# Kernel tuning notes

Measured on AMD Instinct MI355X. Metric: run time of the kernel, lower is better.

Reference implementation:

```python
import jax, jax.numpy as jnp
import numpy as np

NUM_EXPERTS = 8
TOP_K = 2
HIDDEN = 1024
INTER = 3584
BATCH = 2
SEQ = 2048
TOKENS = BATCH * SEQ


def setup_inputs() -> dict:
    key = jax.random.key(0)
    k_h, k_l, k_w1, k_w2, k_w3 = jax.random.split(key, 5)
    hidden_states = jax.random.normal(k_h, (TOKENS, HIDDEN), dtype=jnp.float32)
    # Router: top-2 over softmaxed logits, renormalized (standard Mixtral routing)
    logits = jax.random.normal(k_l, (TOKENS, NUM_EXPERTS), dtype=jnp.float32)
    probs = jax.nn.softmax(logits, axis=-1)
    routing_weights, selected = jax.lax.top_k(probs, TOP_K)  # [T, K], [T, K]
    routing_weights = routing_weights / jnp.sum(routing_weights, axis=-1, keepdims=True)
    # expert_mask: [num_experts, top_k, tokens]
    expert_mask = jax.nn.one_hot(selected, NUM_EXPERTS, dtype=jnp.int32).transpose(2, 1, 0)
    scale = 0.02
    w1 = jax.random.normal(k_w1, (NUM_EXPERTS, HIDDEN, INTER), dtype=jnp.float32) * scale
    w2 = jax.random.normal(k_w2, (NUM_EXPERTS, INTER, HIDDEN), dtype=jnp.float32) * scale
    w3 = jax.random.normal(k_w3, (NUM_EXPERTS, HIDDEN, INTER), dtype=jnp.float32) * scale
    return {
        "expert_mask": expert_mask,
        "hidden_states": hidden_states,
        "routing_weights": routing_weights,
        "w1": w1,
        "w2": w2,
        "w3": w3,
        "batch_size": BATCH,
        "sequence_length": SEQ,
        "hidden_dim": HIDDEN,
    }


def reference(expert_mask, hidden_states, routing_weights, w1, w2, w3,
              batch_size, sequence_length, hidden_dim):
    num_experts = w1.shape[0]
    tokens = batch_size * sequence_length
    # Extra row at the end absorbs writes from fill_value=-1 padding (as in source).
    final = jnp.zeros((tokens + 1, hidden_dim), dtype=hidden_states.dtype)
    for e in range(num_experts):
        # idx: which top-k slot; top_x: which token. Padded with -1.
        idx, top_x = jnp.nonzero(expert_mask[e], size=sequence_length, fill_value=-1)
        cur = hidden_states[top_x]  # [S, H]
        h = (jax.nn.silu(cur @ w1[e]) * (cur @ w3[e])) @ w2[e]  # SwiGLU MLP
        h = h * routing_weights[top_x, idx, None]
        final = final.at[top_x].set(h + final[top_x])
    final = final[:-1]
    return final.reshape(batch_size, sequence_length, hidden_dim)
```

## Files before the change

### kernel.cpp

```cpp
#include <hip/hip_runtime.h>
#include <hip/hip_bf16.h>
#include <cstdint>
#include <cstddef>

#define NEXP  8
#define NTOK  4096
#define HID   1024
#define INTER 3584
#define CAP   2048

#define BM  128
#define BN  128
#define BK  32
#define BKP 40

typedef __attribute__((ext_vector_type(4))) float floatx4;
typedef __attribute__((ext_vector_type(8))) short shortx8;

__device__ __forceinline__ unsigned short f2bf(float f) {
    union { float f; unsigned u; } v; v.f = f;
    unsigned r = v.u + 0x7fffu + ((v.u >> 16) & 1u);
    return (unsigned short)(r >> 16);
}

__device__ __forceinline__ shortx8 pack8(const float* v) {
    shortx8 r;
#pragma unroll
    for (int i = 0; i < 8; ++i) r[i] = (short)f2bf(v[i]);
    return r;
}

__global__ void route_kernel(const int* __restrict__ mask, const float* __restrict__ rw,
                             int* __restrict__ cnt, int* __restrict__ list,
                             float* __restrict__ wgt) {
    int t = blockIdx.x * blockDim.x + threadIdx.x;
    if (t >= NTOK) return;
#pragma unroll
    for (int e = 0; e < NEXP; ++e) {
#pragma unroll
        for (int k = 0; k < 2; ++k) {
            if (mask[(e * 2 + k) * NTOK + t] != 0) {
                int pos = atomicAdd(&cnt[e], 1);
                if (pos < CAP) {
                    list[e * CAP + pos] = t;
                    wgt[e * CAP + pos] = rw[t * 2 + k];
                }
            }
        }
    }
}

__global__ __launch_bounds__(256, 2)
void gemm1_kernel(const float* __restrict__ X, const float* __restrict__ W1,
                  const float* __restrict__ W3, const int* __restrict__ cnt,
                  const int* __restrict__ list, const float* __restrict__ wgt,
                  unsigned short* __restrict__ H) {
    const int e  = blockIdx.z;
    const int ce = min(cnt[e], CAP);
    const int m0 = blockIdx.y * BM;
    if (m0 >= ce) return;
    const int n0 = blockIdx.x * BN;

    __shared__ unsigned short lds_a [BM * BKP];
    __shared__ unsigned short lds_w1[BN * BKP];
    __shared__ unsigned short lds_w3[BN * BKP];

    const int tid = threadIdx.x;
    const int am = tid >> 1;
    const int ah = tid & 1;
    const int tok = list[e * CAP + min(m0 + am, ce - 1)];
    const float* xp = X + (size_t)tok * HID;
    const int wn = tid & 127;
    const int wk = tid >> 7;
    const float* w1base = W1 + (size_t)e * HID * INTER + n0 + wn;
    const float* w3base = W3 + (size_t)e * HID * INTER + n0 + wn;

    const int lane = tid & 63;
    const int wave = tid >> 6;
    const int wm  = (wave >> 1) * 64;
    const int wnn = (wave & 1) * 64;
    const int fl  = lane & 15;
    const int fq  = lane >> 4;

    floatx4 acc1[4][4], acc3[4][4];
#pragma unroll
    for (int i = 0; i < 4; ++i)
#pragma unroll
        for (int j = 0; j < 4; ++j)
#pragma unroll
            for (int r = 0; r < 4; ++r) { acc1[i][j][r] = 0.f; acc3[i][j][r] = 0.f; }

    for (int k0 = 0; k0 < HID; k0 += BK) {
        __syncthreads();
        {
            const float* s = xp + k0 + ah * 16;
            float v[16];
#pragma unroll
            for (int i = 0; i < 4; ++i) {
                float4 f = ((const float4*)s)[i];
                v[4*i+0]=f.x; v[4*i+1]=f.y; v[4*i+2]=f.z; v[4*i+3]=f.w;
            }
            shortx8* dst = (shortx8*)&lds_a[am * BKP + ah * 16];
            dst[0] = pack8(v);
            dst[1] = pack8(v + 8);
        }
#pragma unroll
        for (int p = 0; p < 2; ++p) {
            const int kk = p * 16 + wk * 8;
            {
                const float* s = w1base + (size_t)(k0 + kk) * INTER;
                float v[8];
#pragma unroll
                for (int i = 0; i < 8; ++i) v[i] = s[(size_t)i * INTER];
                *(shortx8*)&lds_w1[wn * BKP + kk] = pack8(v);
            }
            {
                const float* s = w3base + (size_t)(k0 + kk) * INTER;
                float v[8];
#pragma unroll
                for (int i = 0; i < 8; ++i) v[i] = s[(size_t)i * INTER];
                *(shortx8*)&lds_w3[wn * BKP + kk] = pack8(v);
            }
        }
        __syncthreads();

        shortx8 af[4], b1[4], b3[4];
#pragma unroll
        for (int i = 0; i < 4; ++i)
            af[i] = *(const shortx8*)&lds_a[(wm + i * 16 + fl) * BKP + fq * 8];
#pragma unroll
        for (int j = 0; j < 4; ++j) {
            b1[j] = *(const shortx8*)&lds_w1[(wnn + j * 16 + fl) * BKP + fq * 8];
            b3[j] = *(const shortx8*)&lds_w3[(wnn + j * 16 + fl) * BKP + fq * 8];
        }
#pragma unroll
        for (int i = 0; i < 4; ++i)
#pragma unroll
            for (int j = 0; j < 4; ++j) {
                acc1[i][j] = __builtin_amdgcn_mfma_f32_16x16x32_bf16(af[i], b1[j], acc1[i][j], 0, 0, 0);
                acc3[i][j] = __builtin_amdgcn_mfma_f32_16x16x32_bf16(af[i], b3[j], acc3[i][j], 0, 0, 0);
            }
    }

#pragma unroll
    for (int i = 0; i < 4; ++i) {
        const int rowb = m0 + wm + i * 16 + fq * 4;
#pragma unroll
        for (int r = 0; r < 4; ++r) {
            const int row = rowb + r;
            const bool valid = row < ce;
            const float rwv = valid ? wgt[e * CAP + row] : 0.f;
            unsigned short* hp = H + (size_t)(e * CAP + (valid ? row : 0)) * INTER;
#pragma unroll
            for (int j = 0; j < 4; ++j) {
                const int col = n0 + wnn + j * 16 + fl;
                float h1 = acc1[i][j][r];
                float h3 = acc3[i][j][r];
                float sv = h1 / (1.f + __expf(-h1)) * h3 * rwv;
                if (valid) hp[col] = f2bf(sv);
            }
        }
    }
}

__global__ __launch_bounds__(256, 2)
void gemm2_kernel(const unsigned short* __restrict__ H, const float* __restrict__ W2,
                  const int* __restrict__ cnt, const int* __restrict__ list,
                  float* __restrict__ out) {
    const int e  = blockIdx.z;
    const int ce = min(cnt[e], CAP);
    const int m0 = blockIdx.y * BM;
    if (m0 >= ce) return;
    const int n0 = blockIdx.x * BN;

    __shared__ unsigned short lds_a[BM * BKP];
    __shared__ unsigned short lds_w[BN * BKP];

    const int tid = threadIdx.x;
    const int am = tid >> 1;
    const int ah = tid & 1;
    const int arow = min(m0 + am, ce - 1);
    const unsigned short* hp = H + (size_t)(e * CAP + arow) * INTER;

    const int wn = tid & 127;
    const int wk = tid >> 7;
    const float* w2base = W2 + (size_t)e * INTER * HID + n0 + wn;

    const int lane = tid & 63;
    const int wave = tid >> 6;
    const int wm  = (wave >> 1) * 64;
    const int wnn = (wave & 1) * 64;
    const int fl  = lane & 15;
    const int fq  = lane >> 4;

    floatx4 acc[4][4];
#pragma unroll
    for (int i = 0; i < 4; ++i)
#pragma unroll
        for (int j = 0; j < 4; ++j)
#pragma unroll
            for (int r = 0; r < 4; ++r) acc[i][j][r] = 0.f;

    for (int k0 = 0; k0 < INTER; k0 += BK) {
        __syncthreads();
        {
            const shortx8* s = (const shortx8*)(hp + k0 + ah * 16);
            shortx8 v0 = s[0], v1 = s[1];
            shortx8* dst = (shortx8*)&lds_a[am * BKP + ah * 16];
            dst[0] = v0; dst[1] = v1;
        }
#pragma unroll
        for (int p = 0; p < 2; ++p) {
            const int kk = p * 16 + wk * 8;
            const float* s = w2base + (size_t)(k0 + kk) * HID;
            float v[8];
#pragma unroll
            for (int i = 0; i < 8; ++i) v[i] = s[(size_t)i * HID];
            *(shortx8*)&lds_w[wn * BKP + kk] = pack8(v);
        }
        __syncthreads();

        shortx8 af[4], bf[4];
#pragma unroll
        for (int i = 0; i < 4; ++i)
            af[i] = *(const shortx8*)&lds_a[(wm + i * 16 + fl) * BKP + fq * 8];
#pragma unroll
        for (int j = 0; j < 4; ++j)
            bf[j] = *(const shortx8*)&lds_w[(wnn + j * 16 + fl) * BKP + fq * 8];
#pragma unroll
        for (int i = 0; i < 4; ++i)
#pragma unroll
            for (int j = 0; j < 4; ++j)
                acc[i][j] = __builtin_amdgcn_mfma_f32_16x16x32_bf16(af[i], bf[j], acc[i][j], 0, 0, 0);
    }

#pragma unroll
    for (int i = 0; i < 4; ++i) {
        const int rowb = m0 + wm + i * 16 + fq * 4;
#pragma unroll
        for (int r = 0; r < 4; ++r) {
            const int row = rowb + r;
            const bool valid = row < ce;
            const int tok = valid ? list[e * CAP + row] : 0;
            float* op = out + (size_t)tok * HID;
#pragma unroll
            for (int j = 0; j < 4; ++j) {
                const int col = n0 + wnn + j * 16 + fl;
                if (valid) atomicAdd(&op[col], acc[i][j][r]);
            }
        }
    }
}

extern "C" void kernel_launch(void* const* d_in, const int* in_sizes, int n_in,
                              void* d_out, int out_size, void* d_ws, size_t ws_size,
                              hipStream_t stream) {
    const int*   mask = (const int*)  d_in[0];
    const float* X    = (const float*)d_in[1];
    const float* rw   = (const float*)d_in[2];
    const float* w1   = (const float*)d_in[3];
    const float* w2   = (const float*)d_in[4];
    const float* w3   = (const float*)d_in[5];
    float* out = (float*)d_out;

    char* ws = (char*)d_ws;
    int*   cnt  = (int*)ws;
    int*   list = (int*)(ws + 256);
    float* wgt  = (float*)(ws + 256 + 65536);
    unsigned short* H = (unsigned short*)(ws + 256 + 131072);

    hipMemsetAsync(cnt, 0, 256, stream);
    hipMemsetAsync(d_out, 0, (size_t)out_size * sizeof(float), stream);

    route_kernel<<<dim3((NTOK + 255) / 256), dim3(256), 0, stream>>>(mask, rw, cnt, list, wgt);
    gemm1_kernel<<<dim3(INTER / BN, CAP / BM, NEXP), dim3(256), 0, stream>>>(X, w1, w3, cnt, list, wgt, H);
    gemm2_kernel<<<dim3(HID / BN, CAP / BM, NEXP), dim3(256), 0, stream>>>(H, w2, cnt, list, out);
}
```

Measured before the change: 762.1 us.

## Pre-convert weights to transposed bf16 and use async global-to-LDS loads

Adds per-call pre-pass kernels that convert X to bf16 and transpose-convert W1, W3 and W2 to K-contiguous bf16 layouts in workspace. Both GEMMs then fill their LDS tiles with 16-byte direct global-to-LDS loads instead of strided fp32 loads followed by in-register conversion. The aim is to halve weight traffic inside the GEMMs and drop the conversion ALU work from their inner loops. In exchange, every call pays a full fp32 read and bf16 write of all weights, and the LDS tiles lose their padding, which may cause bank conflicts.

```diff
diff --git a/kernel.cpp b/kernel.cpp
--- a/kernel.cpp
+++ b/kernel.cpp
@@ -12,15 +12,15 @@
 #define BM  128
 #define BN  128
 #define BK  32
-#define BKP 40
 
 typedef __attribute__((ext_vector_type(4))) float floatx4;
 typedef __attribute__((ext_vector_type(8))) short shortx8;
-
-__device__ __forceinline__ unsigned short f2bf(float f) {
+typedef unsigned short u16;
+
+__device__ __forceinline__ u16 f2bf(float f) {
     union { float f; unsigned u; } v; v.f = f;
     unsigned r = v.u + 0x7fffu + ((v.u >> 16) & 1u);
-    return (unsigned short)(r >> 16);
+    return (u16)(r >> 16);
 }
 
 __device__ __forceinline__ shortx8 pack8(const float* v) {
@@ -28,6 +28,12 @@
 #pragma unroll
     for (int i = 0; i < 8; ++i) r[i] = (short)f2bf(v[i]);
     return r;
+}
+
+__device__ __forceinline__ void async_ld16(const void* g, void* l) {
+    __builtin_amdgcn_global_load_lds(
+        (const __attribute__((address_space(1))) unsigned int*)g,
+        (__attribute__((address_space(3))) unsigned int*)l, 16, 0, 0);
 }
 
 __global__ void route_kernel(const int* __restrict__ mask, const float* __restrict__ rw,
@@ -50,37 +56,82 @@
     }
 }
 
+__global__ void xcvt_kernel(const float* __restrict__ X, u16* __restrict__ Xb) {
+    const int i = (blockIdx.x * 256 + threadIdx.x) * 8;
+    float4 a = *(const float4*)&X[i];
+    float4 b = *(const float4*)&X[i + 4];
+    float v[8] = {a.x, a.y, a.z, a.w, b.x, b.y, b.z, b.w};
+    *(shortx8*)&Xb[i] = pack8(v);
+}
+
+__global__ void transpose_cvt_kernel(const float* __restrict__ src, u16* __restrict__ dst,
+                                     int K, int N) {
+    const int e = blockIdx.z;
+    src += (size_t)e * K * N;
+    dst += (size_t)e * K * N;
+    const int n0 = blockIdx.x * 64;
+    const int k0 = blockIdx.y * 64;
+    __shared__ u16 lds[64 * 72];
+    const int t  = threadIdx.x;
+    const int rr = t >> 4;
+    const int c4 = t & 15;
+#pragma unroll
+    for (int it = 0; it < 4; ++it) {
+        const int r = it * 16 + rr;
+        float4 f = *(const float4*)&src[(size_t)(k0 + r) * N + n0 + c4 * 4];
+        lds[(c4 * 4 + 0) * 72 + r] = f2bf(f.x);
+        lds[(c4 * 4 + 1) * 72 + r] = f2bf(f.y);
+        lds[(c4 * 4 + 2) * 72 + r] = f2bf(f.z);
+        lds[(c4 * 4 + 3) * 72 + r] = f2bf(f.w);
+    }
+    __syncthreads();
+    const int row8 = t >> 3;
+    const int col8 = t & 7;
+#pragma unroll
+    for (int it = 0; it < 2; ++it) {
+        const int row = it * 32 + row8;
+        *(shortx8*)&dst[(size_t)(n0 + row) * K + k0 + col8 * 8] =
+            *(const shortx8*)&lds[row * 72 + col8 * 8];
+    }
+}
+
 __global__ __launch_bounds__(256, 2)
-void gemm1_kernel(const float* __restrict__ X, const float* __restrict__ W1,
-                  const float* __restrict__ W3, const int* __restrict__ cnt,
+void gemm1_kernel(const u16* __restrict__ Xb, const u16* __restrict__ W1b,
+                  const u16* __restrict__ W3b, const int* __restrict__ cnt,
                   const int* __restrict__ list, const float* __restrict__ wgt,
-                  unsigned short* __restrict__ H) {
+                  u16* __restrict__ H) {
     const int e  = blockIdx.z;
     const int ce = min(cnt[e], CAP);
     const int m0 = blockIdx.y * BM;
     if (m0 >= ce) return;
     const int n0 = blockIdx.x * BN;
 
-    __shared__ unsigned short lds_a [BM * BKP];
-    __shared__ unsigned short lds_w1[BN * BKP];
-    __shared__ unsigned short lds_w3[BN * BKP];
-
-    const int tid = threadIdx.x;
-    const int am = tid >> 1;
-    const int ah = tid & 1;
-    const int tok = list[e * CAP + min(m0 + am, ce - 1)];
-    const float* xp = X + (size_t)tok * HID;
-    const int wn = tid & 127;
-    const int wk = tid >> 7;
-    const float* w1base = W1 + (size_t)e * HID * INTER + n0 + wn;
-    const float* w3base = W3 + (size_t)e * HID * INTER + n0 + wn;
-
+    __shared__ u16 lA [BM * BK];
+    __shared__ u16 lB1[BN * BK];
+    __shared__ u16 lB3[BN * BK];
+
+    const int tid  = threadIdx.x;
     const int lane = tid & 63;
     const int wave = tid >> 6;
+
+    const int srow0 = wave * 32 + (lane >> 2);
+    const int srow1 = srow0 + 16;
+    const int scol  = (lane & 3) * 8;
+    const int lo0 = wave * 1024 + lane * 8;
+    const int lo1 = lo0 + 512;
+
+    const int t0 = list[e * CAP + min(m0 + srow0, ce - 1)];
+    const int t1 = list[e * CAP + min(m0 + srow1, ce - 1)];
+    const u16* ap0  = Xb + (size_t)t0 * HID + scol;
+    const u16* ap1  = Xb + (size_t)t1 * HID + scol;
+    const u16* b1p0 = W1b + ((size_t)e * INTER + n0 + srow0) * HID + scol;
+    const u16* b1p1 = b1p0 + (size_t)16 * HID;
+    const u16* b3p0 = W3b + ((size_t)e * INTER + n0 + srow0) * HID + scol;
+    const u16* b3p1 = b3p0 + (size_t)16 * HID;
+
+    const int fl = lane & 15, fq = lane >> 4;
     const int wm  = (wave >> 1) * 64;
     const int wnn = (wave & 1) * 64;
-    const int fl  = lane & 15;
-    const int fq  = lane >> 4;
 
     floatx4 acc1[4][4], acc3[4][4];
 #pragma unroll
@@ -92,53 +143,29 @@
 
     for (int k0 = 0; k0 < HID; k0 += BK) {
         __syncthreads();
-        {
-            const float* s = xp + k0 + ah * 16;
-            float v[16];
-#pragma unroll
-            for (int i = 0; i < 4; ++i) {
-                float4 f = ((const float4*)s)[i];
-                v[4*i+0]=f.x; v[4*i+1]=f.y; v[4*i+2]=f.z; v[4*i+3]=f.w;
-            }
-            shortx8* dst = (shortx8*)&lds_a[am * BKP + ah * 16];
-            dst[0] = pack8(v);
-            dst[1] = pack8(v + 8);
+        async_ld16(ap0  + k0, &lA [lo0]);
+        async_ld16(ap1  + k0, &lA [lo1]);
+        async_ld16(b1p0 + k0, &lB1[lo0]);
+        async_ld16(b1p1 + k0, &lB1[lo1]);
+        async_ld16(b3p0 + k0, &lB3[lo0]);
+        async_ld16(b3p1 + k0, &lB3[lo1]);
+        __syncthreads();
+
+        shortx8 af[4], b1f[4], b3f[4];
+#pragma unroll
+        for (int i = 0; i < 4; ++i)
+            af[i] = *(const shortx8*)&lA[(wm + i * 16 + fl) * BK + fq * 8];
+#pragma unroll
+        for (int j = 0; j < 4; ++j) {
+            b1f[j] = *(const shortx8*)&lB1[(wnn + j * 16 + fl) * BK + fq * 8];
+            b3f[j] = *(const shortx8*)&lB3[(wnn + j * 16 + fl) * BK + fq * 8];
         }
 #pragma unroll
-        for (int p = 0; p < 2; ++p) {
-            const int kk = p * 16 + wk * 8;
-            {
-                const float* s = w1base + (size_t)(k0 + kk) * INTER;
-                float v[8];
-#pragma unroll
-                for (int i = 0; i < 8; ++i) v[i] = s[(size_t)i * INTER];
-                *(shortx8*)&lds_w1[wn * BKP + kk] = pack8(v);
-            }
-            {
-                const float* s = w3base + (size_t)(k0 + kk) * INTER;
-                float v[8];
-#pragma unroll
-                for (int i = 0; i < 8; ++i) v[i] = s[(size_t)i * INTER];
-                *(shortx8*)&lds_w3[wn * BKP + kk] = pack8(v);
-            }
-        }
-        __syncthreads();
-
-        shortx8 af[4], b1[4], b3[4];
-#pragma unroll
         for (int i = 0; i < 4; ++i)
-            af[i] = *(const shortx8*)&lds_a[(wm + i * 16 + fl) * BKP + fq * 8];
-#pragma unroll
-        for (int j = 0; j < 4; ++j) {
-            b1[j] = *(const shortx8*)&lds_w1[(wnn + j * 16 + fl) * BKP + fq * 8];
-            b3[j] = *(const shortx8*)&lds_w3[(wnn + j * 16 + fl) * BKP + fq * 8];
-        }
-#pragma unroll
-        for (int i = 0; i < 4; ++i)
 #pragma unroll
             for (int j = 0; j < 4; ++j) {
-                acc1[i][j] = __builtin_amdgcn_mfma_f32_16x16x32_bf16(af[i], b1[j], acc1[i][j], 0, 0, 0);
-                acc3[i][j] = __builtin_amdgcn_mfma_f32_16x16x32_bf16(af[i], b3[j], acc3[i][j], 0, 0, 0);
+                acc1[i][j] = __builtin_amdgcn_mfma_f32_16x16x32_bf16(af[i], b1f[j], acc1[i][j], 0, 0, 0);
+                acc3[i][j] = __builtin_amdgcn_mfma_f32_16x16x32_bf16(af[i], b3f[j], acc3[i][j], 0, 0, 0);
             }
     }
 
@@ -150,7 +177,7 @@
             const int row = rowb + r;
             const bool valid = row < ce;
             const float rwv = valid ? wgt[e * CAP + row] : 0.f;
-            unsigned short* hp = H + (size_t)(e * CAP + (valid ? row : 0)) * INTER;
+            u16* hp = H + (size_t)(e * CAP + (valid ? row : 0)) * INTER;
 #pragma unroll
             for (int j = 0; j < 4; ++j) {
                 const int col = n0 + wnn + j * 16 + fl;
@@ -164,7 +191,7 @@
 }
 
 __global__ __launch_bounds__(256, 2)
-void gemm2_kernel(const unsigned short* __restrict__ H, const float* __restrict__ W2,
+void gemm2_kernel(const u16* __restrict__ H, const u16* __restrict__ W2b,
                   const int* __restrict__ cnt, const int* __restrict__ list,
                   float* __restrict__ out) {
     const int e  = blockIdx.z;
@@ -173,25 +200,27 @@
     if (m0 >= ce) return;
     const int n0 = blockIdx.x * BN;
 
-    __shared__ unsigned short lds_a[BM * BKP];
-    __shared__ unsigned short lds_w[BN * BKP];
-
-    const int tid = threadIdx.x;
-    const int am = tid >> 1;
-    const int ah = tid & 1;
-    const int arow = min(m0 + am, ce - 1);
-    const unsigned short* hp = H + (size_t)(e * CAP + arow) * INTER;
-
-    const int wn = tid & 127;
-    const int wk = tid >> 7;
-    const float* w2base = W2 + (size_t)e * INTER * HID + n0 + wn;
-
+    __shared__ u16 lA[BM * BK];
+    __shared__ u16 lB[BN * BK];
+
+    const int tid  = threadIdx.x;
     const int lane = tid & 63;
     const int wave = tid >> 6;
+
+    const int srow0 = wave * 32 + (lane >> 2);
+    const int srow1 = srow0 + 16;
+    const int scol  = (lane & 3) * 8;
+    const int lo0 = wave * 1024 + lane * 8;
+    const int lo1 = lo0 + 512;
+
+    const u16* ap0 = H + (size_t)(e * CAP + m0 + srow0) * INTER + scol;
+    const u16* ap1 = ap0 + (size_t)16 * INTER;
+    const u16* bp0 = W2b + ((size_t)e * HID + n0 + srow0) * INTER + scol;
+    const u16* bp1 = bp0 + (size_t)16 * INTER;
+
+    const int fl = lane & 15, fq = lane >> 4;
     const int wm  = (wave >> 1) * 64;
     const int wnn = (wave & 1) * 64;
-    const int fl  = lane & 15;
-    const int fq  = lane >> 4;
 
     floatx4 acc[4][4];
 #pragma unroll
@@ -203,30 +232,19 @@
 
     for (int k0 = 0; k0 < INTER; k0 += BK) {
         __syncthreads();
-        {
-            const shortx8* s = (const shortx8*)(hp + k0 + ah * 16);
-            shortx8 v0 = s[0], v1 = s[1];
-            shortx8* dst = (shortx8*)&lds_a[am * BKP + ah * 16];
-            dst[0] = v0; dst[1] = v1;
-        }
-#pragma unroll
-        for (int p = 0; p < 2; ++p) {
-            const int kk = p * 16 + wk * 8;
-            const float* s = w2base + (size_t)(k0 + kk) * HID;
-            float v[8];
-#pragma unroll
-            for (int i = 0; i < 8; ++i) v[i] = s[(size_t)i * HID];
-            *(shortx8*)&lds_w[wn * BKP + kk] = pack8(v);
-        }
+        async_ld16(ap0 + k0, &lA[lo0]);
+        async_ld16(ap1 + k0, &lA[lo1]);
+        async_ld16(bp0 + k0, &lB[lo0]);
+        async_ld16(bp1 + k0, &lB[lo1]);
         __syncthreads();
 
         shortx8 af[4], bf[4];
 #pragma unroll
         for (int i = 0; i < 4; ++i)
-            af[i] = *(const shortx8*)&lds_a[(wm + i * 16 + fl) * BKP + fq * 8];
+            af[i] = *(const shortx8*)&lA[(wm + i * 16 + fl) * BK + fq * 8];
 #pragma unroll
         for (int j = 0; j < 4; ++j)
-            bf[j] = *(const shortx8*)&lds_w[(wnn + j * 16 + fl) * BKP + fq * 8];
+            bf[j] = *(const shortx8*)&lB[(wnn + j * 16 + fl) * BK + fq * 8];
 #pragma unroll
         for (int i = 0; i < 4; ++i)
 #pragma unroll
@@ -264,15 +282,25 @@
     float* out = (float*)d_out;
 
     char* ws = (char*)d_ws;
-    int*   cnt  = (int*)ws;
-    int*   list = (int*)(ws + 256);
-    float* wgt  = (float*)(ws + 256 + 65536);
-    unsigned short* H = (unsigned short*)(ws + 256 + 131072);
+    size_t off = 0;
+    int*   cnt  = (int*)(ws + off);  off += 256;
+    int*   list = (int*)(ws + off);  off += (size_t)NEXP * CAP * 4;
+    float* wgt  = (float*)(ws + off); off += (size_t)NEXP * CAP * 4;
+    u16*   Xb   = (u16*)(ws + off);  off += (size_t)NTOK * HID * 2;
+    u16*   W1b  = (u16*)(ws + off);  off += (size_t)NEXP * HID * INTER * 2;
+    u16*   W3b  = (u16*)(ws + off);  off += (size_t)NEXP * HID * INTER * 2;
+    u16*   W2b  = (u16*)(ws + off);  off += (size_t)NEXP * HID * INTER * 2;
+    u16*   H    = (u16*)(ws + off);  off += (size_t)NEXP * CAP * INTER * 2;
 
     hipMemsetAsync(cnt, 0, 256, stream);
     hipMemsetAsync(d_out, 0, (size_t)out_size * sizeof(float), stream);
 
     route_kernel<<<dim3((NTOK + 255) / 256), dim3(256), 0, stream>>>(mask, rw, cnt, list, wgt);
-    gemm1_kernel<<<dim3(INTER / BN, CAP / BM, NEXP), dim3(256), 0, stream>>>(X, w1, w3, cnt, list, wgt, H);
-    gemm2_kernel<<<dim3(HID / BN, CAP / BM, NEXP), dim3(256), 0, stream>>>(H, w2, cnt, list, out);
-}
+    xcvt_kernel<<<dim3(NTOK * HID / (256 * 8)), dim3(256), 0, stream>>>(X, Xb);
+    transpose_cvt_kernel<<<dim3(INTER / 64, HID / 64, NEXP), dim3(256), 0, stream>>>(w1, W1b, HID, INTER);
+    transpose_cvt_kernel<<<dim3(INTER / 64, HID / 64, NEXP), dim3(256), 0, stream>>>(w3, W3b, HID, INTER);
+    transpose_cvt_kernel<<<dim3(HID / 64, INTER / 64, NEXP), dim3(256), 0, stream>>>(w2, W2b, INTER, HID);
+
+    gemm1_kernel<<<dim3(INTER / BN, CAP / BM, NEXP), dim3(256), 0, stream>>>(Xb, W1b, W3b, cnt, list, wgt, H);
+    gemm2_kernel<<<dim3(HID / BN, CAP / BM, NEXP), dim3(256), 0, stream>>>(H, W2b, cnt, list, out);
+}
```

New measurement: 722.8 us. 5.2% less time.
